# Kernel optimization log

Hardware: AMD Instinct MI355X
Metric: run time of the kernel (lower is better)

The kernel has to match this reference:

```python
import jax, jax.numpy as jnp
import numpy as np

LN_EPS = 1e-5

def _layernorm(x, gamma, beta):
    m = jnp.mean(x, axis=-1, keepdims=True)
    v = jnp.mean(jnp.square(x - m), axis=-1, keepdims=True)
    return (x - m) * jax.lax.rsqrt(v + LN_EPS) * gamma + beta

def setup_inputs() -> dict:
    N, D, B = 100000, 64, 512
    key = jax.random.key(0)
    k0, k1, k2, k3, k4, k5, k6 = jax.random.split(key, 7)
    query_place_ids = jax.random.randint(k0, (B,), 0, N)
    Eo = jax.random.normal(k1, (N, D), dtype=jnp.float32) * 0.02
    Ed = jax.random.normal(k2, (N, D), dtype=jnp.float32) * 0.02
    gamma_o = 1.0 + 0.01 * jax.random.normal(k3, (D,), dtype=jnp.float32)
    beta_o = 0.01 * jax.random.normal(k4, (D,), dtype=jnp.float32)
    gamma_d = 1.0 + 0.01 * jax.random.normal(k5, (D,), dtype=jnp.float32)
    beta_d = 0.01 * jax.random.normal(k6, (D,), dtype=jnp.float32)
    return {"query_place_ids": query_place_ids, "Eo": Eo, "Ed": Ed,
            "gamma_o": gamma_o, "beta_o": beta_o,
            "gamma_d": gamma_d, "beta_d": beta_d}

def reference(query_place_ids, Eo, Ed, gamma_o, beta_o, gamma_d, beta_d):
    # Dropout is inference-mode identity. LayerNorm is per-row, so
    # normalizing the full table then gathering equals gather-then-LN.
    # The torch expand()+bmm is mathematically a single shared GEMM
    # [B,D] x [D,N]; we express it that way (the fusion target).
    Co = _layernorm(Eo, gamma_o, beta_o)              # [N, D]
    Cd = _layernorm(Ed, gamma_d, beta_d)              # [N, D]
    q_out = Co[query_place_ids]                       # [B, D] (o-emb of queries)
    q_in = Cd[query_place_ids]                        # [B, D] (d-emb of queries)
    outflow_trans_weight = jax.nn.softmax(jnp.einsum('bd,nd->bn', q_out, Cd), axis=-1)
    inflow_trans_weight = jax.nn.softmax(jnp.einsum('bd,nd->bn', q_in, Co), axis=-1)
    return (outflow_trans_weight, inflow_trans_weight)
```

## Files before the change

### kernel.cpp

```cpp
#include <hip/hip_runtime.h>

typedef _Float16 half8 __attribute__((ext_vector_type(8)));
typedef float floatx4 __attribute__((ext_vector_type(4)));

#define DDIM 64
#define LN_EPS 1e-5f
#define SHIFT 20.0f

#define RB 128
#define CK 64
#define CPB 8
#define STR 72

__device__ inline float wave_sum(float v) {
#pragma unroll
  for (int m = 1; m < 64; m <<= 1) v += __shfl_xor(v, m, 64);
  return v;
}

__global__ __launch_bounds__(256) void ln_kernel(
    const float* __restrict__ Eo, const float* __restrict__ Ed,
    const float* __restrict__ go, const float* __restrict__ bo,
    const float* __restrict__ gd, const float* __restrict__ bd,
    _Float16* __restrict__ Co_hi, _Float16* __restrict__ Co_lo,
    _Float16* __restrict__ Cd_hi, _Float16* __restrict__ Cd_lo, int N) {
  int row = blockIdx.x * 4 + (threadIdx.x >> 6);
  if (row >= N) return;
  int lane = threadIdx.x & 63;
  size_t idx = (size_t)row * DDIM + lane;
  {
    float x = Eo[idx];
    float m = wave_sum(x) * (1.0f / DDIM);
    float d = x - m;
    float var = wave_sum(d * d) * (1.0f / DDIM);
    float y = d * rsqrtf(var + LN_EPS) * go[lane] + bo[lane];
    _Float16 hi = (_Float16)y;
    Co_hi[idx] = hi;
    Co_lo[idx] = (_Float16)(y - (float)hi);
  }
  {
    float x = Ed[idx];
    float m = wave_sum(x) * (1.0f / DDIM);
    float d = x - m;
    float var = wave_sum(d * d) * (1.0f / DDIM);
    float y = d * rsqrtf(var + LN_EPS) * gd[lane] + bd[lane];
    _Float16 hi = (_Float16)y;
    Cd_hi[idx] = hi;
    Cd_lo[idx] = (_Float16)(y - (float)hi);
  }
}

template <int PASS>
__global__ __launch_bounds__(256, 2) void score_kernel(
    const _Float16* __restrict__ Co_hi, const _Float16* __restrict__ Co_lo,
    const _Float16* __restrict__ Cd_hi, const _Float16* __restrict__ Cd_lo,
    const int* __restrict__ ids, float* __restrict__ sums,
    float* __restrict__ out, int N, int B) {
  __shared__ __attribute__((aligned(16))) _Float16 Qh[RB * STR];
  __shared__ __attribute__((aligned(16))) _Float16 Ql[RB * STR];
  __shared__ __attribute__((aligned(16))) _Float16 Ch[CK * STR];
  __shared__ __attribute__((aligned(16))) _Float16 Cl[CK * STR];
  __shared__ float inv_lds[RB];

  const int t = threadIdx.x;
  const int mat = blockIdx.z;
  const int mbase = blockIdx.y * RB;
  const _Float16* Qsrc_h = (mat == 0) ? Co_hi : Cd_hi;
  const _Float16* Qsrc_l = (mat == 0) ? Co_lo : Cd_lo;
  const _Float16* Csrc_h = (mat == 0) ? Cd_hi : Co_hi;
  const _Float16* Csrc_l = (mat == 0) ? Cd_lo : Co_lo;

#pragma unroll
  for (int rnd = 0; rnd < 4; ++rnd) {
    int f = (rnd * 256 + t) * 16;
    int r = f >> 7;
    int off = f & 127;
    int id = ids[mbase + r];
    *(uint4*)((char*)Qh + r * (STR * 2) + off) =
        *(const uint4*)((const char*)Qsrc_h + (size_t)id * 128 + off);
    *(uint4*)((char*)Ql + r * (STR * 2) + off) =
        *(const uint4*)((const char*)Qsrc_l + (size_t)id * 128 + off);
  }
  if (PASS == 1) {
    if (t < RB) inv_lds[t] = 1.0f / sums[(size_t)mat * B + mbase + t];
  }
  __syncthreads();

  const int lane = t & 63;
  const int wv = t >> 6;
  const int l15 = lane & 15;
  const int quad = lane >> 4;

  half8 Ah[2][2], Al[2][2];
#pragma unroll
  for (int mt = 0; mt < 2; ++mt) {
    int r = wv * 32 + mt * 16 + l15;
    int e0 = r * STR + quad * 8;
    Ah[mt][0] = *(const half8*)&Qh[e0];
    Ah[mt][1] = *(const half8*)&Qh[e0 + 32];
    Al[mt][0] = *(const half8*)&Ql[e0];
    Al[mt][1] = *(const half8*)&Ql[e0 + 32];
  }

  float sumacc[2][4];
  if (PASS == 0) {
#pragma unroll
    for (int mt = 0; mt < 2; ++mt)
#pragma unroll
      for (int r = 0; r < 4; ++r) sumacc[mt][r] = 0.0f;
  }

  const int nc_total = (N + CK - 1) / CK;
  const int c0 = blockIdx.x * CPB;
  for (int ic = 0; ic < CPB; ++ic) {
    int chunk = c0 + ic;
    if (chunk >= nc_total) break;
    int nbase = chunk * CK;
    __syncthreads();
#pragma unroll
    for (int rnd = 0; rnd < 2; ++rnd) {
      int f = (rnd * 256 + t) * 16;
      int r = f >> 7;
      int off = f & 127;
      int grow = nbase + r;
      if (grow < N) {
        *(uint4*)((char*)Ch + r * (STR * 2) + off) =
            *(const uint4*)((const char*)Csrc_h + (size_t)grow * 128 + off);
        *(uint4*)((char*)Cl + r * (STR * 2) + off) =
            *(const uint4*)((const char*)Csrc_l + (size_t)grow * 128 + off);
      } else {
        uint4 z = {0, 0, 0, 0};
        *(uint4*)((char*)Ch + r * (STR * 2) + off) = z;
        *(uint4*)((char*)Cl + r * (STR * 2) + off) = z;
      }
    }
    __syncthreads();

#pragma unroll
    for (int nt = 0; nt < 4; ++nt) {
      int cr = nt * 16 + l15;
      int e0 = cr * STR + quad * 8;
      half8 Bh0 = *(const half8*)&Ch[e0];
      half8 Bh1 = *(const half8*)&Ch[e0 + 32];
      half8 Bl0 = *(const half8*)&Cl[e0];
      half8 Bl1 = *(const half8*)&Cl[e0 + 32];
      int col = nbase + nt * 16 + l15;
      bool valid = col < N;
#pragma unroll
      for (int mt = 0; mt < 2; ++mt) {
        floatx4 acc = {0.0f, 0.0f, 0.0f, 0.0f};
        acc = __builtin_amdgcn_mfma_f32_16x16x32_f16(Ah[mt][0], Bh0, acc, 0, 0, 0);
        acc = __builtin_amdgcn_mfma_f32_16x16x32_f16(Ah[mt][1], Bh1, acc, 0, 0, 0);
        acc = __builtin_amdgcn_mfma_f32_16x16x32_f16(Ah[mt][0], Bl0, acc, 0, 0, 0);
        acc = __builtin_amdgcn_mfma_f32_16x16x32_f16(Ah[mt][1], Bl1, acc, 0, 0, 0);
        acc = __builtin_amdgcn_mfma_f32_16x16x32_f16(Al[mt][0], Bh0, acc, 0, 0, 0);
        acc = __builtin_amdgcn_mfma_f32_16x16x32_f16(Al[mt][1], Bh1, acc, 0, 0, 0);
#pragma unroll
        for (int r = 0; r < 4; ++r) {
          float p = __expf(acc[r] - SHIFT);
          if (PASS == 0) {
            sumacc[mt][r] += valid ? p : 0.0f;
          } else if (valid) {
            int rl = wv * 32 + mt * 16 + quad * 4 + r;
            int b = mbase + rl;
            out[(size_t)mat * B * N + (size_t)b * N + col] = p * inv_lds[rl];
          }
        }
      }
    }
  }

  if (PASS == 0) {
#pragma unroll
    for (int mt = 0; mt < 2; ++mt)
#pragma unroll
      for (int r = 0; r < 4; ++r) {
        float v = sumacc[mt][r];
        v += __shfl_xor(v, 1, 64);
        v += __shfl_xor(v, 2, 64);
        v += __shfl_xor(v, 4, 64);
        v += __shfl_xor(v, 8, 64);
        if (l15 == 0) {
          int rl = wv * 32 + mt * 16 + quad * 4 + r;
          atomicAdd(&sums[(size_t)mat * B + mbase + rl], v);
        }
      }
  }
}

extern "C" void kernel_launch(void* const* d_in, const int* in_sizes, int n_in,
                              void* d_out, int out_size, void* d_ws, size_t ws_size,
                              hipStream_t stream) {
  const int* ids = (const int*)d_in[0];
  const float* Eo = (const float*)d_in[1];
  const float* Ed = (const float*)d_in[2];
  const float* go = (const float*)d_in[3];
  const float* bo = (const float*)d_in[4];
  const float* gd = (const float*)d_in[5];
  const float* bd = (const float*)d_in[6];
  const int B = in_sizes[0];
  const int N = in_sizes[1] / DDIM;
  float* out = (float*)d_out;

  char* ws = (char*)d_ws;
  size_t plane = (size_t)N * DDIM * sizeof(_Float16);
  _Float16* Co_hi = (_Float16*)(ws + 0 * plane);
  _Float16* Co_lo = (_Float16*)(ws + 1 * plane);
  _Float16* Cd_hi = (_Float16*)(ws + 2 * plane);
  _Float16* Cd_lo = (_Float16*)(ws + 3 * plane);
  float* sums = (float*)(ws + 4 * plane);

  hipMemsetAsync(sums, 0, (size_t)2 * B * sizeof(float), stream);

  ln_kernel<<<(N + 3) / 4, 256, 0, stream>>>(Eo, Ed, go, bo, gd, bd,
                                             Co_hi, Co_lo, Cd_hi, Cd_lo, N);

  int nc_total = (N + CK - 1) / CK;
  int gx = (nc_total + CPB - 1) / CPB;
  dim3 grid(gx, B / RB, 2);
  score_kernel<0><<<grid, 256, 0, stream>>>(Co_hi, Co_lo, Cd_hi, Cd_lo, ids,
                                            sums, out, N, B);
  score_kernel<1><<<grid, 256, 0, stream>>>(Co_hi, Co_lo, Cd_hi, Cd_lo, ids,
                                            sums, out, N, B);
}
```

Before: 592.5 us.

## Fuse score passes, write unnormalized probs, rescale; double-buffer chunks via direct-to-LDS loads

The two score passes (sum pass, then write pass) are merged into one pass that writes unnormalized exp values while accumulating row sums, and a separate rescale kernel then divides the output in place. Column chunks are loaded straight into a double-buffered, XOR-swizzled LDS tile with global_load_lds and explicit vmcnt waits, using a persistent grid of 192 blocks that strides over chunks. This removes the second GEMM and exp recomputation and hides load latency. In exchange, the large output must be read and written a second time by the rescale kernel, and the hand-counted vmcnt values are fragile.

```diff
diff --git a/kernel.cpp b/kernel.cpp
--- a/kernel.cpp
+++ b/kernel.cpp
@@ -9,13 +9,17 @@
 
 #define RB 128
 #define CK 64
-#define CPB 8
-#define STR 72
 
 __device__ inline float wave_sum(float v) {
 #pragma unroll
   for (int m = 1; m < 64; m <<= 1) v += __shfl_xor(v, m, 64);
   return v;
+}
+
+__device__ inline void gld16(const void* g, void* l) {
+  __builtin_amdgcn_global_load_lds(
+      (const __attribute__((address_space(1))) void*)g,
+      (__attribute__((address_space(3))) void*)l, 16, 0, 0);
 }
 
 __global__ __launch_bounds__(256) void ln_kernel(
@@ -50,17 +54,12 @@
   }
 }
 
-template <int PASS>
 __global__ __launch_bounds__(256, 2) void score_kernel(
     const _Float16* __restrict__ Co_hi, const _Float16* __restrict__ Co_lo,
     const _Float16* __restrict__ Cd_hi, const _Float16* __restrict__ Cd_lo,
     const int* __restrict__ ids, float* __restrict__ sums,
-    float* __restrict__ out, int N, int B) {
-  __shared__ __attribute__((aligned(16))) _Float16 Qh[RB * STR];
-  __shared__ __attribute__((aligned(16))) _Float16 Ql[RB * STR];
-  __shared__ __attribute__((aligned(16))) _Float16 Ch[CK * STR];
-  __shared__ __attribute__((aligned(16))) _Float16 Cl[CK * STR];
-  __shared__ float inv_lds[RB];
+    float* __restrict__ out, int N, int B, int nc_total) {
+  __shared__ __attribute__((aligned(16))) _Float16 Cb[2][2][CK * DDIM];
 
   const int t = threadIdx.x;
   const int mat = blockIdx.z;
@@ -70,80 +69,99 @@
   const _Float16* Csrc_h = (mat == 0) ? Cd_hi : Co_hi;
   const _Float16* Csrc_l = (mat == 0) ? Cd_lo : Co_lo;
 
+  const int lane = t & 63;
+  const int wv = t >> 6;
+  const int l15 = lane & 15;
+  const int quad = lane >> 4;
+
+  _Float16* Qh_lds = &Cb[0][0][0];
+  _Float16* Ql_lds = &Cb[1][0][0];
 #pragma unroll
   for (int rnd = 0; rnd < 4; ++rnd) {
     int f = (rnd * 256 + t) * 16;
     int r = f >> 7;
     int off = f & 127;
+    int swoff = off ^ ((r & 7) << 4);
     int id = ids[mbase + r];
-    *(uint4*)((char*)Qh + r * (STR * 2) + off) =
+    *(uint4*)((char*)Qh_lds + r * 128 + swoff) =
         *(const uint4*)((const char*)Qsrc_h + (size_t)id * 128 + off);
-    *(uint4*)((char*)Ql + r * (STR * 2) + off) =
+    *(uint4*)((char*)Ql_lds + r * 128 + swoff) =
         *(const uint4*)((const char*)Qsrc_l + (size_t)id * 128 + off);
   }
-  if (PASS == 1) {
-    if (t < RB) inv_lds[t] = 1.0f / sums[(size_t)mat * B + mbase + t];
-  }
   __syncthreads();
-
-  const int lane = t & 63;
-  const int wv = t >> 6;
-  const int l15 = lane & 15;
-  const int quad = lane >> 4;
 
   half8 Ah[2][2], Al[2][2];
 #pragma unroll
   for (int mt = 0; mt < 2; ++mt) {
     int r = wv * 32 + mt * 16 + l15;
-    int e0 = r * STR + quad * 8;
-    Ah[mt][0] = *(const half8*)&Qh[e0];
-    Ah[mt][1] = *(const half8*)&Qh[e0 + 32];
-    Al[mt][0] = *(const half8*)&Ql[e0];
-    Al[mt][1] = *(const half8*)&Ql[e0 + 32];
-  }
+    int sw = (r & 7) << 4;
+    const char* qh = (const char*)Qh_lds + r * 128;
+    const char* ql = (const char*)Ql_lds + r * 128;
+    Ah[mt][0] = *(const half8*)(qh + ((quad * 16) ^ sw));
+    Ah[mt][1] = *(const half8*)(qh + ((64 + quad * 16) ^ sw));
+    Al[mt][0] = *(const half8*)(ql + ((quad * 16) ^ sw));
+    Al[mt][1] = *(const half8*)(ql + ((64 + quad * 16) ^ sw));
+  }
+  __syncthreads();
+
+  auto stage = [&](int chunk, int buf) {
+    int nbase = chunk * CK;
+    #pragma unroll
+    for (int j = 0; j < 2; ++j) {
+      int slot = wv * 128 + j * 64 + lane;
+      int r = slot >> 3;
+      int gr = nbase + r;
+      if (gr > N - 1) gr = N - 1;
+      int gb = (slot & 7) ^ (r & 7);
+      size_t goff = (size_t)gr * 128 + (size_t)(gb * 16);
+      _Float16* dh = &Cb[buf][0][(wv * 128 + j * 64) * 8];
+      _Float16* dl = &Cb[buf][1][(wv * 128 + j * 64) * 8];
+      gld16((const char*)Csrc_h + goff, dh);
+      gld16((const char*)Csrc_l + goff, dl);
+    }
+  };
 
   float sumacc[2][4];
-  if (PASS == 0) {
-#pragma unroll
-    for (int mt = 0; mt < 2; ++mt)
-#pragma unroll
-      for (int r = 0; r < 4; ++r) sumacc[mt][r] = 0.0f;
-  }
-
-  const int nc_total = (N + CK - 1) / CK;
-  const int c0 = blockIdx.x * CPB;
-  for (int ic = 0; ic < CPB; ++ic) {
-    int chunk = c0 + ic;
-    if (chunk >= nc_total) break;
-    int nbase = chunk * CK;
-    __syncthreads();
-#pragma unroll
-    for (int rnd = 0; rnd < 2; ++rnd) {
-      int f = (rnd * 256 + t) * 16;
-      int r = f >> 7;
-      int off = f & 127;
-      int grow = nbase + r;
-      if (grow < N) {
-        *(uint4*)((char*)Ch + r * (STR * 2) + off) =
-            *(const uint4*)((const char*)Csrc_h + (size_t)grow * 128 + off);
-        *(uint4*)((char*)Cl + r * (STR * 2) + off) =
-            *(const uint4*)((const char*)Csrc_l + (size_t)grow * 128 + off);
-      } else {
-        uint4 z = {0, 0, 0, 0};
-        *(uint4*)((char*)Ch + r * (STR * 2) + off) = z;
-        *(uint4*)((char*)Cl + r * (STR * 2) + off) = z;
-      }
-    }
-    __syncthreads();
-
+#pragma unroll
+  for (int mt = 0; mt < 2; ++mt)
+#pragma unroll
+    for (int r = 0; r < 4; ++r) sumacc[mt][r] = 0.0f;
+
+  const int bx = blockIdx.x;
+  const int gxd = gridDim.x;
+  int nck = (bx < nc_total) ? ((nc_total - 1 - bx) / gxd + 1) : 0;
+  float* orow = out + (size_t)mat * B * N + (size_t)mbase * N;
+
+  if (nck > 0) stage(bx, 0);
+
+  for (int k = 0; k < nck; ++k) {
+    int cur = k & 1;
+    bool pf = (k + 1 < nck);
+    if (pf) stage(bx + (k + 1) * gxd, cur ^ 1);
+    if (k == 0) {
+      if (pf) asm volatile("s_waitcnt vmcnt(4)" ::: "memory");
+      else    asm volatile("s_waitcnt vmcnt(0)" ::: "memory");
+    } else {
+      if (pf) asm volatile("s_waitcnt vmcnt(36)" ::: "memory");
+      else    asm volatile("s_waitcnt vmcnt(32)" ::: "memory");
+    }
+    __builtin_amdgcn_sched_barrier(0);
+    __builtin_amdgcn_s_barrier();
+    __builtin_amdgcn_sched_barrier(0);
+
+    int nbase = (bx + k * gxd) * CK;
+    const _Float16* ChL = &Cb[cur][0][0];
+    const _Float16* ClL = &Cb[cur][1][0];
 #pragma unroll
     for (int nt = 0; nt < 4; ++nt) {
       int cr = nt * 16 + l15;
-      int e0 = cr * STR + quad * 8;
-      half8 Bh0 = *(const half8*)&Ch[e0];
-      half8 Bh1 = *(const half8*)&Ch[e0 + 32];
-      half8 Bl0 = *(const half8*)&Cl[e0];
-      half8 Bl1 = *(const half8*)&Cl[e0 + 32];
+      int sw = (cr & 7) << 4;
+      const char* bh = (const char*)ChL + cr * 128;
+      const char* bl = (const char*)ClL + cr * 128;
+      half8 Bh0 = *(const half8*)(bh + ((quad * 16) ^ sw));
+      half8 Bh1 = *(const half8*)(bh + ((64 + quad * 16) ^ sw));
+      half8 Bl0 = *(const half8*)(bl + ((quad * 16) ^ sw));
+      half8 Bl1 = *(const half8*)(bl + ((64 + quad * 16) ^ sw));
       int col = nbase + nt * 16 + l15;
       bool valid = col < N;
 #pragma unroll
@@ -158,33 +176,50 @@
 #pragma unroll
         for (int r = 0; r < 4; ++r) {
           float p = __expf(acc[r] - SHIFT);
-          if (PASS == 0) {
-            sumacc[mt][r] += valid ? p : 0.0f;
-          } else if (valid) {
+          p = valid ? p : 0.0f;
+          sumacc[mt][r] += p;
+          if (valid) {
             int rl = wv * 32 + mt * 16 + quad * 4 + r;
-            int b = mbase + rl;
-            out[(size_t)mat * B * N + (size_t)b * N + col] = p * inv_lds[rl];
+            orow[(size_t)rl * N + col] = p;
           }
         }
       }
     }
-  }
-
-  if (PASS == 0) {
-#pragma unroll
-    for (int mt = 0; mt < 2; ++mt)
-#pragma unroll
-      for (int r = 0; r < 4; ++r) {
-        float v = sumacc[mt][r];
-        v += __shfl_xor(v, 1, 64);
-        v += __shfl_xor(v, 2, 64);
-        v += __shfl_xor(v, 4, 64);
-        v += __shfl_xor(v, 8, 64);
-        if (l15 == 0) {
-          int rl = wv * 32 + mt * 16 + quad * 4 + r;
-          atomicAdd(&sums[(size_t)mat * B + mbase + rl], v);
-        }
+    __builtin_amdgcn_sched_barrier(0);
+    __builtin_amdgcn_s_barrier();
+  }
+
+#pragma unroll
+  for (int mt = 0; mt < 2; ++mt)
+#pragma unroll
+    for (int r = 0; r < 4; ++r) {
+      float v = sumacc[mt][r];
+      v += __shfl_xor(v, 1, 64);
+      v += __shfl_xor(v, 2, 64);
+      v += __shfl_xor(v, 4, 64);
+      v += __shfl_xor(v, 8, 64);
+      if (l15 == 0) {
+        int rl = wv * 32 + mt * 16 + quad * 4 + r;
+        atomicAdd(&sums[(size_t)mat * B + mbase + rl], v);
       }
+    }
+}
+
+__global__ __launch_bounds__(256) void rescale_kernel(
+    float* __restrict__ out, const float* __restrict__ sums, int N) {
+  int row = blockIdx.y;
+  float inv = 1.0f / sums[row];
+  float4* po = (float4*)(out + (size_t)row * N);
+  int nf4 = N >> 2;
+  for (int i = blockIdx.x * blockDim.x + threadIdx.x; i < nf4;
+       i += gridDim.x * blockDim.x) {
+    float4 v = po[i];
+    v.x *= inv; v.y *= inv; v.z *= inv; v.w *= inv;
+    po[i] = v;
+  }
+  if ((N & 3) && blockIdx.x == 0 && threadIdx.x < (N & 3)) {
+    int idx = (nf4 << 2) + threadIdx.x;
+    out[(size_t)row * N + idx] *= inv;
   }
 }
 
@@ -216,10 +251,10 @@
                                              Co_hi, Co_lo, Cd_hi, Cd_lo, N);
 
   int nc_total = (N + CK - 1) / CK;
-  int gx = (nc_total + CPB - 1) / CPB;
-  dim3 grid(gx, B / RB, 2);
-  score_kernel<0><<<grid, 256, 0, stream>>>(Co_hi, Co_lo, Cd_hi, Cd_lo, ids,
-                                            sums, out, N, B);
-  score_kernel<1><<<grid, 256, 0, stream>>>(Co_hi, Co_lo, Cd_hi, Cd_lo, ids,
-                                            sums, out, N, B);
-}
+  dim3 sgrid(192, B / RB, 2);
+  score_kernel<<<sgrid, 256, 0, stream>>>(Co_hi, Co_lo, Cd_hi, Cd_lo, ids,
+                                          sums, out, N, B, nc_total);
+
+  dim3 rgrid(8, 2 * B);
+  rescale_kernel<<<rgrid, 256, 0, stream>>>(out, sums, N);
+}
```

New measurement: 727.8 us. +22.8%, slower.

## Shrink score kernel LDS, use persistent strided grid and nontemporal output stores

Applied to the files above, without the earlier changes.

The score kernel now reuses one shared buffer for the query hi/lo planes and the column chunk, which cuts LDS from about 46KB to about 18KB, and raises the occupancy hint to 3 blocks per SIMD. The grid becomes a fixed 96x4x2 persistent layout where each block walks column chunks with a grid stride, in place of 8 consecutive chunks per block. Output writes use nontemporal stores, and the row normalisers are held in registers. Trade-offs: extra barriers per chunk, fewer total blocks, and tail rows are clamped instead of zero-filled, which may change load balance.

```diff
diff --git a/kernel.cpp b/kernel.cpp
--- a/kernel.cpp
+++ b/kernel.cpp
@@ -9,8 +9,9 @@
 
 #define RB 128
 #define CK 64
-#define CPB 8
 #define STR 72
+#define ROWB (STR * 2)
+#define PLB (CK * ROWB)
 
 __device__ inline float wave_sum(float v) {
 #pragma unroll
@@ -51,15 +52,12 @@
 }
 
 template <int PASS>
-__global__ __launch_bounds__(256, 2) void score_kernel(
+__global__ __launch_bounds__(256, 3) void score_kernel(
     const _Float16* __restrict__ Co_hi, const _Float16* __restrict__ Co_lo,
     const _Float16* __restrict__ Cd_hi, const _Float16* __restrict__ Cd_lo,
     const int* __restrict__ ids, float* __restrict__ sums,
-    float* __restrict__ out, int N, int B) {
-  __shared__ __attribute__((aligned(16))) _Float16 Qh[RB * STR];
-  __shared__ __attribute__((aligned(16))) _Float16 Ql[RB * STR];
-  __shared__ __attribute__((aligned(16))) _Float16 Ch[CK * STR];
-  __shared__ __attribute__((aligned(16))) _Float16 Cl[CK * STR];
+    float* __restrict__ out, int N, int B, int nc_total) {
+  __shared__ __attribute__((aligned(16))) char Sbuf[2 * PLB];
   __shared__ float inv_lds[RB];
 
   const int t = threadIdx.x;
@@ -70,68 +68,85 @@
   const _Float16* Csrc_h = (mat == 0) ? Cd_hi : Co_hi;
   const _Float16* Csrc_l = (mat == 0) ? Cd_lo : Co_lo;
 
-#pragma unroll
-  for (int rnd = 0; rnd < 4; ++rnd) {
-    int f = (rnd * 256 + t) * 16;
-    int r = f >> 7;
-    int off = f & 127;
-    int id = ids[mbase + r];
-    *(uint4*)((char*)Qh + r * (STR * 2) + off) =
-        *(const uint4*)((const char*)Qsrc_h + (size_t)id * 128 + off);
-    *(uint4*)((char*)Ql + r * (STR * 2) + off) =
-        *(const uint4*)((const char*)Qsrc_l + (size_t)id * 128 + off);
-  }
-  if (PASS == 1) {
-    if (t < RB) inv_lds[t] = 1.0f / sums[(size_t)mat * B + mbase + t];
-  }
-  __syncthreads();
-
   const int lane = t & 63;
   const int wv = t >> 6;
   const int l15 = lane & 15;
   const int quad = lane >> 4;
 
+  if (PASS == 1 && t < RB)
+    inv_lds[t] = 1.0f / sums[(size_t)mat * B + mbase + t];
+
+#pragma unroll
+  for (int j = 0; j < 4; ++j) {
+    int f = (j * 256 + t) * 16;
+    int r = f >> 7;
+    int off = f & 127;
+    int id = ids[mbase + r];
+    *(uint4*)(Sbuf + r * ROWB + off) =
+        *(const uint4*)((const char*)Qsrc_h + (size_t)id * 128 + off);
+  }
+  __syncthreads();
   half8 Ah[2][2], Al[2][2];
 #pragma unroll
   for (int mt = 0; mt < 2; ++mt) {
     int r = wv * 32 + mt * 16 + l15;
-    int e0 = r * STR + quad * 8;
-    Ah[mt][0] = *(const half8*)&Qh[e0];
-    Ah[mt][1] = *(const half8*)&Qh[e0 + 32];
-    Al[mt][0] = *(const half8*)&Ql[e0];
-    Al[mt][1] = *(const half8*)&Ql[e0 + 32];
-  }
+    const char* q = Sbuf + r * ROWB + quad * 16;
+    Ah[mt][0] = *(const half8*)q;
+    Ah[mt][1] = *(const half8*)(q + 64);
+  }
+  float invr[2][4];
+  if (PASS == 1) {
+#pragma unroll
+    for (int mt = 0; mt < 2; ++mt)
+#pragma unroll
+      for (int r2 = 0; r2 < 4; ++r2)
+        invr[mt][r2] = inv_lds[wv * 32 + mt * 16 + quad * 4 + r2];
+  }
+  __syncthreads();
+#pragma unroll
+  for (int j = 0; j < 4; ++j) {
+    int f = (j * 256 + t) * 16;
+    int r = f >> 7;
+    int off = f & 127;
+    int id = ids[mbase + r];
+    *(uint4*)(Sbuf + r * ROWB + off) =
+        *(const uint4*)((const char*)Qsrc_l + (size_t)id * 128 + off);
+  }
+  __syncthreads();
+#pragma unroll
+  for (int mt = 0; mt < 2; ++mt) {
+    int r = wv * 32 + mt * 16 + l15;
+    const char* q = Sbuf + r * ROWB + quad * 16;
+    Al[mt][0] = *(const half8*)q;
+    Al[mt][1] = *(const half8*)(q + 64);
+  }
+  __syncthreads();
 
   float sumacc[2][4];
-  if (PASS == 0) {
-#pragma unroll
-    for (int mt = 0; mt < 2; ++mt)
-#pragma unroll
-      for (int r = 0; r < 4; ++r) sumacc[mt][r] = 0.0f;
-  }
-
-  const int nc_total = (N + CK - 1) / CK;
-  const int c0 = blockIdx.x * CPB;
-  for (int ic = 0; ic < CPB; ++ic) {
-    int chunk = c0 + ic;
-    if (chunk >= nc_total) break;
-    int nbase = chunk * CK;
-    __syncthreads();
-#pragma unroll
-    for (int rnd = 0; rnd < 2; ++rnd) {
-      int f = (rnd * 256 + t) * 16;
-      int r = f >> 7;
-      int off = f & 127;
-      int grow = nbase + r;
-      if (grow < N) {
-        *(uint4*)((char*)Ch + r * (STR * 2) + off) =
-            *(const uint4*)((const char*)Csrc_h + (size_t)grow * 128 + off);
-        *(uint4*)((char*)Cl + r * (STR * 2) + off) =
-            *(const uint4*)((const char*)Csrc_l + (size_t)grow * 128 + off);
-      } else {
-        uint4 z = {0, 0, 0, 0};
-        *(uint4*)((char*)Ch + r * (STR * 2) + off) = z;
-        *(uint4*)((char*)Cl + r * (STR * 2) + off) = z;
+#pragma unroll
+  for (int mt = 0; mt < 2; ++mt)
+#pragma unroll
+    for (int r2 = 0; r2 < 4; ++r2) sumacc[mt][r2] = 0.0f;
+
+  const int bx = blockIdx.x;
+  const int gxd = gridDim.x;
+  int nck = (bx < nc_total) ? ((nc_total - 1 - bx) / gxd + 1) : 0;
+  float* orow = out + (size_t)mat * B * N + (size_t)mbase * N;
+
+  for (int k = 0; k < nck; ++k) {
+    int nbase = (bx + k * gxd) * CK;
+#pragma unroll
+    for (int p = 0; p < 2; ++p) {
+      const char* src = (p == 0) ? (const char*)Csrc_h : (const char*)Csrc_l;
+#pragma unroll
+      for (int j = 0; j < 2; ++j) {
+        int f = (j * 256 + t) * 16;
+        int r = f >> 7;
+        int off = f & 127;
+        int gr = nbase + r;
+        if (gr > N - 1) gr = N - 1;
+        *(uint4*)(Sbuf + p * PLB + r * ROWB + off) =
+            *(const uint4*)(src + (size_t)gr * 128 + off);
       }
     }
     __syncthreads();
@@ -139,11 +154,12 @@
 #pragma unroll
     for (int nt = 0; nt < 4; ++nt) {
       int cr = nt * 16 + l15;
-      int e0 = cr * STR + quad * 8;
-      half8 Bh0 = *(const half8*)&Ch[e0];
-      half8 Bh1 = *(const half8*)&Ch[e0 + 32];
-      half8 Bl0 = *(const half8*)&Cl[e0];
-      half8 Bl1 = *(const half8*)&Cl[e0 + 32];
+      const char* bh = Sbuf + cr * ROWB + quad * 16;
+      const char* bl = bh + PLB;
+      half8 Bh0 = *(const half8*)bh;
+      half8 Bh1 = *(const half8*)(bh + 64);
+      half8 Bl0 = *(const half8*)bl;
+      half8 Bl1 = *(const half8*)(bl + 64);
       int col = nbase + nt * 16 + l15;
       bool valid = col < N;
 #pragma unroll
@@ -156,32 +172,33 @@
         acc = __builtin_amdgcn_mfma_f32_16x16x32_f16(Al[mt][0], Bh0, acc, 0, 0, 0);
         acc = __builtin_amdgcn_mfma_f32_16x16x32_f16(Al[mt][1], Bh1, acc, 0, 0, 0);
 #pragma unroll
-        for (int r = 0; r < 4; ++r) {
-          float p = __expf(acc[r] - SHIFT);
+        for (int r2 = 0; r2 < 4; ++r2) {
+          float p = __expf(acc[r2] - SHIFT);
           if (PASS == 0) {
-            sumacc[mt][r] += valid ? p : 0.0f;
+            sumacc[mt][r2] += valid ? p : 0.0f;
           } else if (valid) {
-            int rl = wv * 32 + mt * 16 + quad * 4 + r;
-            int b = mbase + rl;
-            out[(size_t)mat * B * N + (size_t)b * N + col] = p * inv_lds[rl];
+            int rl = wv * 32 + mt * 16 + quad * 4 + r2;
+            __builtin_nontemporal_store(p * invr[mt][r2],
+                                        &orow[(size_t)rl * N + col]);
           }
         }
       }
     }
+    __syncthreads();
   }
 
   if (PASS == 0) {
 #pragma unroll
     for (int mt = 0; mt < 2; ++mt)
 #pragma unroll
-      for (int r = 0; r < 4; ++r) {
-        float v = sumacc[mt][r];
+      for (int r2 = 0; r2 < 4; ++r2) {
+        float v = sumacc[mt][r2];
         v += __shfl_xor(v, 1, 64);
         v += __shfl_xor(v, 2, 64);
         v += __shfl_xor(v, 4, 64);
         v += __shfl_xor(v, 8, 64);
         if (l15 == 0) {
-          int rl = wv * 32 + mt * 16 + quad * 4 + r;
+          int rl = wv * 32 + mt * 16 + quad * 4 + r2;
           atomicAdd(&sums[(size_t)mat * B + mbase + rl], v);
         }
       }
@@ -216,10 +233,9 @@
                                              Co_hi, Co_lo, Cd_hi, Cd_lo, N);
 
   int nc_total = (N + CK - 1) / CK;
-  int gx = (nc_total + CPB - 1) / CPB;
-  dim3 grid(gx, B / RB, 2);
-  score_kernel<0><<<grid, 256, 0, stream>>>(Co_hi, Co_lo, Cd_hi, Cd_lo, ids,
-                                            sums, out, N, B);
-  score_kernel<1><<<grid, 256, 0, stream>>>(Co_hi, Co_lo, Cd_hi, Cd_lo, ids,
-                                            sums, out, N, B);
-}
+  dim3 sgrid(96, B / RB, 2);
+  score_kernel<0><<<sgrid, 256, 0, stream>>>(Co_hi, Co_lo, Cd_hi, Cd_lo, ids,
+                                             sums, out, N, B, nc_total);
+  score_kernel<1><<<sgrid, 256, 0, stream>>>(Co_hi, Co_lo, Cd_hi, Cd_lo, ids,
+                                             sums, out, N, B, nc_total);
+}
```

New measurement: 584.2 us. No clear change (-1.4%).
